# Kernel optimization log

Measured on AMD Instinct MI355X. Metric: run time of the kernel, lower is better.

## Reference

```python
import jax, jax.numpy as jnp
import numpy as np

NEG_SLOPE = 0.2


def gat_conv(x, src, dst, N, W, a_src, a_dst, b, concat):
    # x: [N, F_in], W: [F_in, H*C], a_src/a_dst: [H, C], b: [H*C] or [C]
    H, C = a_src.shape
    h = (x @ W).reshape(N, H, C)                    # [N, H, C]
    al_src = jnp.einsum('nhc,hc->nh', h, a_src)     # [N, H]
    al_dst = jnp.einsum('nhc,hc->nh', h, a_dst)     # [N, H]
    logits = jax.nn.leaky_relu(al_src[src] + al_dst[dst], NEG_SLOPE)  # [E, H]
    # edge softmax over incoming edges of each destination node
    m = jax.ops.segment_max(logits, dst, num_segments=N)              # [N, H]
    m = jnp.where(jnp.isfinite(m), m, 0.0)
    e = jnp.exp(logits - m[dst])                                      # [E, H]
    denom = jax.ops.segment_sum(e, dst, num_segments=N)               # [N, H]
    alpha = e / denom[dst]                                            # [E, H]
    out = jax.ops.segment_sum(alpha[:, :, None] * h[src], dst, num_segments=N)  # [N, H, C]
    if concat:
        return out.reshape(N, H * C) + b
    return out.mean(axis=1) + b


def setup_inputs() -> dict:
    key = jax.random.key(0)
    ks = jax.random.split(key, 12)
    N, E = 100000, 1600000
    F_in, Ch, Co, H = 128, 32, 64, 4
    x = jax.random.normal(ks[0], (N, F_in), dtype=jnp.float32)
    edge_index = jax.random.randint(ks[1], (2, E), 0, N, dtype=jnp.int64)
    s = 0.1
    return {
        'x': x, 'edge_index': edge_index,
        'W1': jax.random.normal(ks[2], (F_in, H * Ch), jnp.float32) * s,
        'a_src1': jax.random.normal(ks[3], (H, Ch), jnp.float32) * s,
        'a_dst1': jax.random.normal(ks[4], (H, Ch), jnp.float32) * s,
        'b1': jnp.zeros((H * Ch,), jnp.float32),
        'W2': jax.random.normal(ks[5], (H * Ch, H * Ch), jnp.float32) * s,
        'a_src2': jax.random.normal(ks[6], (H, Ch), jnp.float32) * s,
        'a_dst2': jax.random.normal(ks[7], (H, Ch), jnp.float32) * s,
        'b2': jnp.zeros((H * Ch,), jnp.float32),
        'W3': jax.random.normal(ks[8], (H * Ch, H * Co), jnp.float32) * s,
        'a_src3': jax.random.normal(ks[9], (H, Co), jnp.float32) * s,
        'a_dst3': jax.random.normal(ks[10], (H, Co), jnp.float32) * s,
        'b3': jnp.zeros((Co,), jnp.float32),
    }


def reference(x, edge_index, W1, a_src1, a_dst1, b1, W2, a_src2, a_dst2, b2, W3, a_src3, a_dst3, b3):
    N = x.shape[0]
    # PyG GATConv default add_self_loops=True
    loop = jnp.arange(N, dtype=edge_index.dtype)
    src = jnp.concatenate([edge_index[0], loop])
    dst = jnp.concatenate([edge_index[1], loop])
    h = gat_conv(x, src, dst, N, W1, a_src1, a_dst1, b1, concat=True)
    h = jax.nn.elu(h)
    h = gat_conv(h, src, dst, N, W2, a_src2, a_dst2, b2, concat=True)
    h = jax.nn.elu(h)
    out = gat_conv(h, src, dst, N, W3, a_src3, a_dst3, b3, concat=False)
    return out
```

## Files before the change

### kernel.cpp

```cpp
#include <hip/hip_runtime.h>


#define NEG_SLOPE 0.2f

typedef __attribute__((ext_vector_type(8))) _Float16 half8v;
typedef __attribute__((ext_vector_type(4))) _Float16 half4v;
typedef __attribute__((ext_vector_type(2))) _Float16 half2v;
typedef __attribute__((ext_vector_type(4))) float f32x4;

__device__ __forceinline__ float lrelu(float v) { return v > 0.f ? v : NEG_SLOPE * v; }

struct hf2 { _Float16 hi, lo; };
__device__ __forceinline__ hf2 split_f16(float f)
{
    hf2 r;
    r.hi = (_Float16)f;
    r.lo = (_Float16)(f - (float)r.hi);
    return r;
}

__global__ void fill_sentinel(float* __restrict__ out, int n)
{
    int i = blockIdx.x * blockDim.x + threadIdx.x;
    if (i < n) out[i] = 1e30f;
}

__global__ void detect_idx64(const int* __restrict__ ei, int* __restrict__ flag)
{
    __shared__ int anynz;
    if (threadIdx.x == 0) anynz = 0;
    __syncthreads();
    int v = ei[2 * threadIdx.x + 1];
    if (v != 0) atomicOr(&anynz, 1);
    __syncthreads();
    if (threadIdx.x == 0) flag[0] = (anynz == 0) ? 1 : 0;
}

__global__ void prep_edges(const void* __restrict__ ei, const int* __restrict__ flag,
                           int* __restrict__ src32, int* __restrict__ dst32,
                           int* __restrict__ deg8, int* __restrict__ loc, int N, int E)
{
    int e = blockIdx.x * blockDim.x + threadIdx.x;
    if (e >= E) return;
    int s, d;
    if (flag[0]) { s = (int)((const long long*)ei)[e]; d = (int)((const long long*)ei)[E + e]; }
    else         { s = ((const int*)ei)[e];            d = ((const int*)ei)[E + e]; }
    src32[e] = s;
    dst32[e] = d;
    loc[e] = atomicAdd(&deg8[(blockIdx.x & 7) * N + d], 1);
}

__global__ void reduce8(int* __restrict__ deg8, int* __restrict__ deg, int N)
{
    int d = blockIdx.x * blockDim.x + threadIdx.x;
    if (d >= N) return;
    int s = 0;
    #pragma unroll
    for (int k = 0; k < 8; ++k) {
        int v = deg8[k * N + d];
        deg8[k * N + d] = s;
        s += v;
    }
    deg[d] = s;
}

__global__ __launch_bounds__(256)
void scanA(const int* __restrict__ deg, int* __restrict__ rowptr,
           int* __restrict__ bsum, int N)
{
    __shared__ int part[256];
    const int t = threadIdx.x;
    const int base = blockIdx.x * 1024 + t * 4;
    int v[4];
    #pragma unroll
    for (int j = 0; j < 4; ++j) v[j] = (base + j < N) ? deg[base + j] : 0;
    int s = v[0] + v[1] + v[2] + v[3];
    part[t] = s;
    __syncthreads();
    #pragma unroll
    for (int off = 1; off < 256; off <<= 1) {
        int p = (t >= off) ? part[t - off] : 0;
        __syncthreads();
        part[t] += p;
        __syncthreads();
    }
    int run = (t == 0) ? 0 : part[t - 1];
    #pragma unroll
    for (int j = 0; j < 4; ++j) {
        if (base + j < N) rowptr[base + j] = run;
        run += v[j];
    }
    if (t == 255) bsum[blockIdx.x] = part[255];
}

__global__ __launch_bounds__(1024)
void scanB(int* __restrict__ bsum, int nb)
{
    __shared__ int s[1024];
    int t = threadIdx.x;
    s[t] = (t < nb) ? bsum[t] : 0;
    __syncthreads();
    for (int off = 1; off < 1024; off <<= 1) {
        int p = (t >= off) ? s[t - off] : 0;
        __syncthreads();
        s[t] += p;
        __syncthreads();
    }
    if (t < nb) bsum[t] = (t == 0) ? 0 : s[t - 1];
}

__global__ __launch_bounds__(256)
void scanC(int* __restrict__ rowptr, const int* __restrict__ bsum, int N, int E)
{
    const int base = blockIdx.x * 1024 + threadIdx.x * 4;
    const int off = bsum[blockIdx.x];
    #pragma unroll
    for (int j = 0; j < 4; ++j)
        if (base + j < N) rowptr[base + j] += off;
    if (blockIdx.x == 0 && threadIdx.x == 0) rowptr[N] = E;
}

__global__ void fill_csr(const int* __restrict__ src32, const int* __restrict__ dst32,
                         const int* __restrict__ loc, const int* __restrict__ rowptr,
                         const int* __restrict__ deg8, int* __restrict__ csr_src,
                         int N, int E)
{
    int e = blockIdx.x * blockDim.x + threadIdx.x;
    if (e >= E) return;
    int d = dst32[e];
    csr_src[rowptr[d] + deg8[(blockIdx.x & 7) * N + d] + loc[e]] = src32[e];
}

__global__ void convert_hilo(const float* __restrict__ in, _Float16* __restrict__ hi,
                             _Float16* __restrict__ lo, long long n4)
{
    long long t = (long long)blockIdx.x * blockDim.x + threadIdx.x;
    if (t >= n4) return;
    float4 v = *(const float4*)&in[t * 4];
    hf2 a = split_f16(v.x), b = split_f16(v.y), c = split_f16(v.z), d = split_f16(v.w);
    half4v h, l;
    h.x = a.hi; h.y = b.hi; h.z = c.hi; h.w = d.hi;
    l.x = a.lo; l.y = b.lo; l.z = c.lo; l.w = d.lo;
    *(half4v*)&hi[t * 4] = h;
    *(half4v*)&lo[t * 4] = l;
}

__global__ __launch_bounds__(256)
void convert_wt(const float* __restrict__ W, _Float16* __restrict__ wthi,
                _Float16* __restrict__ wtlo, int ldw, int wcol0)
{
    int t = blockIdx.x * 256 + threadIdx.x;
    int k = t >> 7, n = t & 127;
    float v = W[(long long)k * ldw + wcol0 + n];
    hf2 r = split_f16(v);
    wthi[n * 128 + k] = r.hi;
    wtlo[n * 128 + k] = r.lo;
}

template<int HPC>
__global__ __launch_bounds__(256)
void gemm_mfma(const _Float16* __restrict__ Ahi, const _Float16* __restrict__ Alo,
               const _Float16* __restrict__ Wthi, const _Float16* __restrict__ Wtlo,
               _Float16* __restrict__ Chi,
               const float* __restrict__ aS, const float* __restrict__ aD,
               float* __restrict__ als, float* __restrict__ ald, int M)
{
    const int tid = threadIdx.x;
    const int wave = tid >> 6, lane = tid & 63;
    const int l15 = lane & 15, lk = lane >> 4;
    const int m0 = blockIdx.x * 64 + wave * 16;
    int mrow = m0 + l15;
    if (mrow >= M) mrow = M - 1;

    f32x4 acc[8];
    #pragma unroll
    for (int i = 0; i < 8; ++i) acc[i] = (f32x4){0.f, 0.f, 0.f, 0.f};

    #pragma unroll
    for (int kt = 0; kt < 4; ++kt) {
        const int k = kt * 32 + lk * 8;
        half8v ah = *(const half8v*)&Ahi[(long long)mrow * 128 + k];
        half8v al = *(const half8v*)&Alo[(long long)mrow * 128 + k];
        #pragma unroll
        for (int nf = 0; nf < 8; ++nf) {
            half8v bh = *(const half8v*)&Wthi[(nf * 16 + l15) * 128 + k];
            half8v bl = *(const half8v*)&Wtlo[(nf * 16 + l15) * 128 + k];
            acc[nf] = __builtin_amdgcn_mfma_f32_16x16x32_f16(ah, bh, acc[nf], 0, 0, 0);
            acc[nf] = __builtin_amdgcn_mfma_f32_16x16x32_f16(ah, bl, acc[nf], 0, 0, 0);
            acc[nf] = __builtin_amdgcn_mfma_f32_16x16x32_f16(al, bh, acc[nf], 0, 0, 0);
        }
    }

    #pragma unroll
    for (int r = 0; r < 4; ++r) {
        int gm = m0 + lk * 4 + r;
        if (gm >= M) continue;
        #pragma unroll
        for (int nf = 0; nf < 8; ++nf)
            Chi[(long long)gm * 128 + nf * 16 + l15] = (_Float16)acc[nf][r];
    }

    float asv[8], adv[8];
    #pragma unroll
    for (int nf = 0; nf < 8; ++nf) {
        asv[nf] = aS[nf * 16 + l15];
        adv[nf] = aD[nf * 16 + l15];
    }
    constexpr int NFH = 8 / HPC;
    #pragma unroll
    for (int r = 0; r < 4; ++r) {
        #pragma unroll
        for (int h = 0; h < HPC; ++h) {
            float ps = 0.f, pd = 0.f;
            #pragma unroll
            for (int q = 0; q < NFH; ++q) {
                int nf = h * NFH + q;
                ps += acc[nf][r] * asv[nf];
                pd += acc[nf][r] * adv[nf];
            }
            #pragma unroll
            for (int m = 1; m < 16; m <<= 1) {
                ps += __shfl_xor(ps, m);
                pd += __shfl_xor(pd, m);
            }
            if (l15 == 0) {
                int gm = m0 + lk * 4 + r;
                if (gm < M) {
                    als[gm * HPC + h] = ps;
                    ald[gm * HPC + h] = pd;
                }
            }
        }
    }
}

template<int C, int HL, bool MEAN, bool ACCUM>
__global__ __launch_bounds__(256)
void gat_aggregate(const int* __restrict__ rowptr, const int* __restrict__ csr_src,
                   const float* __restrict__ als, const float* __restrict__ ald,
                   const _Float16* __restrict__ h16, const float* __restrict__ bias,
                   float* __restrict__ out,
                   _Float16* __restrict__ ohi, _Float16* __restrict__ olo, int N)
{
    constexpr int ROW = HL * C;
    constexpr int LOG2HL = (HL == 4) ? 2 : 1;
    const int d = (blockIdx.x * blockDim.x + threadIdx.x) >> 6;
    const int lane = threadIdx.x & 63;
    if (d >= N) return;
    const int j = lane * 2;
    const int hh = j / C;

    const int myh = lane & (HL - 1);
    const int myi = lane >> LOG2HL;
    const float ald_mine = ald[d * HL + myh];

    const float ald_d = (HL == 4 && myh == hh) ? ald_mine : ald[d * HL + hh];
    const float wself = __expf(lrelu(als[d * HL + hh] + ald_d));
    float denom = wself;
    half2v hv = *(const half2v*)&h16[(unsigned)d * ROW + j];
    float vx = wself * (float)hv.x, vy = wself * (float)hv.y;

    const int e0 = rowptr[d], e1 = rowptr[d + 1];
    for (int base = e0; base < e1; base += 8) {
        int ee = base + myi;
        int sv_mine = csr_src[ee < e1 ? ee : e1 - 1];
        float a = als[sv_mine * HL + myh] + ald_mine;
        float w_mine = (ee < e1) ? __expf(lrelu(a)) : 0.f;

        int sref[8];
        half2v hb[8];
        #pragma unroll
        for (int i = 0; i < 8; ++i) sref[i] = __shfl(sv_mine, i * HL, 64);
        #pragma unroll
        for (int i = 0; i < 8; ++i) hb[i] = *(const half2v*)&h16[(unsigned)sref[i] * ROW + j];
        #pragma unroll
        for (int i = 0; i < 8; ++i) {
            float wv = __shfl(w_mine, i * HL + hh, 64);
            denom += wv;
            vx += wv * (float)hb[i].x;
            vy += wv * (float)hb[i].y;
        }
    }
    float inv = 1.f / denom;
    vx *= inv; vy *= inv;

    if (!MEAN) {
        vx += bias[j]; vy += bias[j + 1];
        vx = vx > 0.f ? vx : __expf(vx) - 1.f;
        vy = vy > 0.f ? vy : __expf(vy) - 1.f;
        hf2 rx = split_f16(vx), ry = split_f16(vy);
        half2v hi2, lo2;
        hi2.x = rx.hi; hi2.y = ry.hi;
        lo2.x = rx.lo; lo2.y = ry.lo;
        *(half2v*)&ohi[(unsigned)d * ROW + j] = hi2;
        *(half2v*)&olo[(unsigned)d * ROW + j] = lo2;
    } else {
        vx = 0.25f * vx + __shfl_xor(0.25f * vx, 32);
        vy = 0.25f * vy + __shfl_xor(0.25f * vy, 32);
        if (lane < 32) {
            float* op = &out[(unsigned)d * C + j];
            if (ACCUM) { vx += op[0] + bias[j]; vy += op[1] + bias[j + 1]; }
            *(float2*)op = make_float2(vx, vy);
        }
    }
}

extern "C" void kernel_launch(void* const* d_in, const int* in_sizes, int n_in,
                              void* d_out, int out_size, void* d_ws, size_t ws_size,
                              hipStream_t stream)
{
    const float* x      = (const float*)d_in[0];
    const void*  ei     = d_in[1];
    const float* W1     = (const float*)d_in[2];
    const float* a_src1 = (const float*)d_in[3];
    const float* a_dst1 = (const float*)d_in[4];
    const float* b1     = (const float*)d_in[5];
    const float* W2     = (const float*)d_in[6];
    const float* a_src2 = (const float*)d_in[7];
    const float* a_dst2 = (const float*)d_in[8];
    const float* b2     = (const float*)d_in[9];
    const float* W3     = (const float*)d_in[10];
    const float* a_src3 = (const float*)d_in[11];
    const float* a_dst3 = (const float*)d_in[12];
    const float* b3     = (const float*)d_in[13];

    const int N = in_sizes[0] / 128;
    const int E = in_sizes[1] / 2;

    char* w = (char*)d_ws;
    auto alloc = [&](size_t bytes) {
        char* p = w;
        w += (bytes + 255) & ~(size_t)255;
        return p;
    };
    int*      flag    = (int*)     alloc(256);
    int*      deg8    = (int*)     alloc((size_t)N * 8 * 4);
    int*      deg     = (int*)     alloc((size_t)N * 4);
    int*      rowptr  = (int*)     alloc((size_t)(N + 1) * 4);
    int*      bsum    = (int*)     alloc(1024 * 4);
    int*      src32   = (int*)     alloc((size_t)E * 4);
    int*      dst32   = (int*)     alloc((size_t)E * 4);
    int*      loc     = (int*)     alloc((size_t)E * 4);
    int*      csr_src = (int*)     alloc((size_t)E * 4);
    _Float16* hhi     = (_Float16*)alloc((size_t)N * 128 * 2);
    _Float16* xhi     = (_Float16*)alloc((size_t)N * 128 * 2);
    _Float16* xlo     = (_Float16*)alloc((size_t)N * 128 * 2);
    float*    als     = (float*)   alloc((size_t)N * 4 * 4);
    float*    ald     = (float*)   alloc((size_t)N * 4 * 4);
    _Float16* wthi    = (_Float16*)alloc(128 * 128 * 2);
    _Float16* wtlo    = (_Float16*)alloc(128 * 128 * 2);
    if ((size_t)(w - (char*)d_ws) > ws_size) {
        fill_sentinel<<<(out_size + 255) / 256, 256, 0, stream>>>((float*)d_out, out_size);
        return;
    }

    const int gb = 256;
    const int nb1024 = (N + 1023) / 1024;
    const int mb = (N + 63) / 64;
    const int ab = (N * 64 + gb - 1) / gb;
    auto blocks = [&](long long tot) { return (int)((tot + gb - 1) / gb); };

    detect_idx64<<<1, 256, 0, stream>>>((const int*)ei, flag);
    (void)hipMemsetAsync(deg8, 0, (size_t)N * 8 * 4, stream);
    prep_edges<<<blocks(E), gb, 0, stream>>>(ei, flag, src32, dst32, deg8, loc, N, E);
    reduce8<<<blocks(N), gb, 0, stream>>>(deg8, deg, N);
    scanA<<<nb1024, gb, 0, stream>>>(deg, rowptr, bsum, N);
    scanB<<<1, 1024, 0, stream>>>(bsum, nb1024);
    scanC<<<nb1024, gb, 0, stream>>>(rowptr, bsum, N, E);
    fill_csr<<<blocks(E), gb, 0, stream>>>(src32, dst32, loc, rowptr, deg8, csr_src, N, E);

    convert_hilo<<<blocks((long long)N * 32), gb, 0, stream>>>(x, xhi, xlo, (long long)N * 32);

    convert_wt<<<64, gb, 0, stream>>>(W1, wthi, wtlo, 128, 0);
    gemm_mfma<4><<<mb, gb, 0, stream>>>(xhi, xlo, wthi, wtlo, hhi,
                                        a_src1, a_dst1, als, ald, N);
    gat_aggregate<32, 4, false, false><<<ab, gb, 0, stream>>>(
        rowptr, csr_src, als, ald, hhi, b1, nullptr, xhi, xlo, N);

    convert_wt<<<64, gb, 0, stream>>>(W2, wthi, wtlo, 128, 0);
    gemm_mfma<4><<<mb, gb, 0, stream>>>(xhi, xlo, wthi, wtlo, hhi,
                                        a_src2, a_dst2, als, ald, N);
    gat_aggregate<32, 4, false, false><<<ab, gb, 0, stream>>>(
        rowptr, csr_src, als, ald, hhi, b2, nullptr, xhi, xlo, N);

    convert_wt<<<64, gb, 0, stream>>>(W3, wthi, wtlo, 256, 0);
    gemm_mfma<2><<<mb, gb, 0, stream>>>(xhi, xlo, wthi, wtlo, hhi,
                                        a_src3, a_dst3, als, ald, N);
    gat_aggregate<64, 2, true, false><<<ab, gb, 0, stream>>>(
        rowptr, csr_src, als, ald, hhi, b3, (float*)d_out, nullptr, nullptr, N);

    convert_wt<<<64, gb, 0, stream>>>(W3, wthi, wtlo, 256, 128);
    gemm_mfma<2><<<mb, gb, 0, stream>>>(xhi, xlo, wthi, wtlo, hhi,
                                        a_src3 + 128, a_dst3 + 128, als, ald, N);
    gat_aggregate<64, 2, true, true><<<ab, gb, 0, stream>>>(
        rowptr, csr_src, als, ald, hhi, b3, (float*)d_out, nullptr, nullptr, N);
}
```

Baseline: 698.8 us.

## Merge layer-3 two-pass head split into single 256-wide GEMM and aggregation

Layer 3 used to run as two half-width passes, each with its own GEMM and aggregation over the edges, accumulating into the output. These become one 256-column MFMA GEMM and one aggregation kernel that handles all four heads, with 4 halves per lane and a cross-lane mean. This removes a second full edge traversal and a second GEMM launch, at the cost of a larger intermediate buffer and more registers per thread. Separately, the edge preprocessing now keys its per-bucket degree counters on the hardware XCC id instead of the block index, encoding the bucket in the top bits of loc. It also uses nontemporal loads and stores for the streaming edge arrays, and restricts the weight computation in the aggregation to the lanes that need it.

```diff
diff --git a/kernel.cpp b/kernel.cpp
--- a/kernel.cpp
+++ b/kernel.cpp
@@ -42,12 +42,21 @@
 {
     int e = blockIdx.x * blockDim.x + threadIdx.x;
     if (e >= E) return;
+    int xcc;
+    asm("s_getreg_b32 %0, hwreg(HW_REG_XCC_ID)" : "=s"(xcc));
+    xcc &= 7;
     int s, d;
-    if (flag[0]) { s = (int)((const long long*)ei)[e]; d = (int)((const long long*)ei)[E + e]; }
-    else         { s = ((const int*)ei)[e];            d = ((const int*)ei)[E + e]; }
-    src32[e] = s;
-    dst32[e] = d;
-    loc[e] = atomicAdd(&deg8[(blockIdx.x & 7) * N + d], 1);
+    if (flag[0]) {
+        s = (int)__builtin_nontemporal_load((const long long*)ei + e);
+        d = (int)__builtin_nontemporal_load((const long long*)ei + E + e);
+    } else {
+        s = __builtin_nontemporal_load((const int*)ei + e);
+        d = __builtin_nontemporal_load((const int*)ei + E + e);
+    }
+    __builtin_nontemporal_store(s, src32 + e);
+    __builtin_nontemporal_store(d, dst32 + e);
+    int v = atomicAdd(&deg8[xcc * N + d], 1);
+    __builtin_nontemporal_store((xcc << 28) | v, loc + e);
 }
 
 __global__ void reduce8(int* __restrict__ deg8, int* __restrict__ deg, int N)
@@ -127,8 +136,11 @@
 {
     int e = blockIdx.x * blockDim.x + threadIdx.x;
     if (e >= E) return;
-    int d = dst32[e];
-    csr_src[rowptr[d] + deg8[(blockIdx.x & 7) * N + d] + loc[e]] = src32[e];
+    int lv = __builtin_nontemporal_load(loc + e);
+    int d  = __builtin_nontemporal_load(dst32 + e);
+    int s  = __builtin_nontemporal_load(src32 + e);
+    int k  = lv >> 28;
+    csr_src[rowptr[d] + deg8[k * N + d] + (lv & 0x0FFFFFFF)] = s;
 }
 
 __global__ void convert_hilo(const float* __restrict__ in, _Float16* __restrict__ hi,
@@ -147,10 +159,10 @@
 
 __global__ __launch_bounds__(256)
 void convert_wt(const float* __restrict__ W, _Float16* __restrict__ wthi,
-                _Float16* __restrict__ wtlo, int ldw, int wcol0)
+                _Float16* __restrict__ wtlo, int ncols, int ldw, int wcol0)
 {
     int t = blockIdx.x * 256 + threadIdx.x;
-    int k = t >> 7, n = t & 127;
+    int k = t / ncols, n = t % ncols;
     float v = W[(long long)k * ldw + wcol0 + n];
     hf2 r = split_f16(v);
     wthi[n * 128 + k] = r.hi;
@@ -234,12 +246,86 @@
     }
 }
 
-template<int C, int HL, bool MEAN, bool ACCUM>
+__global__ __launch_bounds__(256)
+void gemm_mfma256(const _Float16* __restrict__ Ahi, const _Float16* __restrict__ Alo,
+                  const _Float16* __restrict__ Wthi, const _Float16* __restrict__ Wtlo,
+                  _Float16* __restrict__ Chi,
+                  const float* __restrict__ aS, const float* __restrict__ aD,
+                  float* __restrict__ als, float* __restrict__ ald, int M)
+{
+    const int tid = threadIdx.x;
+    const int wave = tid >> 6, lane = tid & 63;
+    const int l15 = lane & 15, lk = lane >> 4;
+    const int m0 = blockIdx.x * 64 + wave * 16;
+    int mrow = m0 + l15;
+    if (mrow >= M) mrow = M - 1;
+
+    f32x4 acc[16];
+    #pragma unroll
+    for (int i = 0; i < 16; ++i) acc[i] = (f32x4){0.f, 0.f, 0.f, 0.f};
+
+    #pragma unroll
+    for (int kt = 0; kt < 4; ++kt) {
+        const int k = kt * 32 + lk * 8;
+        half8v ah = *(const half8v*)&Ahi[(long long)mrow * 128 + k];
+        half8v al = *(const half8v*)&Alo[(long long)mrow * 128 + k];
+        #pragma unroll
+        for (int nf = 0; nf < 16; ++nf) {
+            half8v bh = *(const half8v*)&Wthi[(nf * 16 + l15) * 128 + k];
+            half8v bl = *(const half8v*)&Wtlo[(nf * 16 + l15) * 128 + k];
+            acc[nf] = __builtin_amdgcn_mfma_f32_16x16x32_f16(ah, bh, acc[nf], 0, 0, 0);
+            acc[nf] = __builtin_amdgcn_mfma_f32_16x16x32_f16(ah, bl, acc[nf], 0, 0, 0);
+            acc[nf] = __builtin_amdgcn_mfma_f32_16x16x32_f16(al, bh, acc[nf], 0, 0, 0);
+        }
+    }
+
+    #pragma unroll
+    for (int r = 0; r < 4; ++r) {
+        int gm = m0 + lk * 4 + r;
+        if (gm >= M) continue;
+        #pragma unroll
+        for (int nf = 0; nf < 16; ++nf)
+            Chi[(long long)gm * 256 + nf * 16 + l15] = (_Float16)acc[nf][r];
+    }
+
+    float asv[16], adv[16];
+    #pragma unroll
+    for (int nf = 0; nf < 16; ++nf) {
+        asv[nf] = aS[nf * 16 + l15];
+        adv[nf] = aD[nf * 16 + l15];
+    }
+    #pragma unroll
+    for (int r = 0; r < 4; ++r) {
+        #pragma unroll
+        for (int h = 0; h < 4; ++h) {
+            float ps = 0.f, pd = 0.f;
+            #pragma unroll
+            for (int q = 0; q < 4; ++q) {
+                int nf = h * 4 + q;
+                ps += acc[nf][r] * asv[nf];
+                pd += acc[nf][r] * adv[nf];
+            }
+            #pragma unroll
+            for (int m = 1; m < 16; m <<= 1) {
+                ps += __shfl_xor(ps, m);
+                pd += __shfl_xor(pd, m);
+            }
+            if (l15 == 0) {
+                int gm = m0 + lk * 4 + r;
+                if (gm < M) {
+                    als[gm * 4 + h] = ps;
+                    ald[gm * 4 + h] = pd;
+                }
+            }
+        }
+    }
+}
+
+template<int C, int HL>
 __global__ __launch_bounds__(256)
 void gat_aggregate(const int* __restrict__ rowptr, const int* __restrict__ csr_src,
                    const float* __restrict__ als, const float* __restrict__ ald,
                    const _Float16* __restrict__ h16, const float* __restrict__ bias,
-                   float* __restrict__ out,
                    _Float16* __restrict__ ohi, _Float16* __restrict__ olo, int N)
 {
     constexpr int ROW = HL * C;
@@ -254,19 +340,21 @@
     const int myi = lane >> LOG2HL;
     const float ald_mine = ald[d * HL + myh];
 
-    const float ald_d = (HL == 4 && myh == hh) ? ald_mine : ald[d * HL + hh];
-    const float wself = __expf(lrelu(als[d * HL + hh] + ald_d));
+    const float wself = __expf(lrelu(als[d * HL + hh] + ald[d * HL + hh]));
     float denom = wself;
     half2v hv = *(const half2v*)&h16[(unsigned)d * ROW + j];
     float vx = wself * (float)hv.x, vy = wself * (float)hv.y;
 
     const int e0 = rowptr[d], e1 = rowptr[d + 1];
     for (int base = e0; base < e1; base += 8) {
-        int ee = base + myi;
-        int sv_mine = csr_src[ee < e1 ? ee : e1 - 1];
-        float a = als[sv_mine * HL + myh] + ald_mine;
-        float w_mine = (ee < e1) ? __expf(lrelu(a)) : 0.f;
-
+        int sv_mine = 0;
+        float w_mine = 0.f;
+        if (lane < 8 * HL) {
+            int ee = base + myi;
+            sv_mine = csr_src[ee < e1 ? ee : e1 - 1];
+            float a = als[sv_mine * HL + myh] + ald_mine;
+            w_mine = (ee < e1) ? __expf(lrelu(a)) : 0.f;
+        }
         int sref[8];
         half2v hb[8];
         #pragma unroll
@@ -282,26 +370,76 @@
         }
     }
     float inv = 1.f / denom;
-    vx *= inv; vy *= inv;
-
-    if (!MEAN) {
-        vx += bias[j]; vy += bias[j + 1];
-        vx = vx > 0.f ? vx : __expf(vx) - 1.f;
-        vy = vy > 0.f ? vy : __expf(vy) - 1.f;
-        hf2 rx = split_f16(vx), ry = split_f16(vy);
-        half2v hi2, lo2;
-        hi2.x = rx.hi; hi2.y = ry.hi;
-        lo2.x = rx.lo; lo2.y = ry.lo;
-        *(half2v*)&ohi[(unsigned)d * ROW + j] = hi2;
-        *(half2v*)&olo[(unsigned)d * ROW + j] = lo2;
-    } else {
-        vx = 0.25f * vx + __shfl_xor(0.25f * vx, 32);
-        vy = 0.25f * vy + __shfl_xor(0.25f * vy, 32);
+    vx = vx * inv + bias[j];
+    vy = vy * inv + bias[j + 1];
+    vx = vx > 0.f ? vx : __expf(vx) - 1.f;
+    vy = vy > 0.f ? vy : __expf(vy) - 1.f;
+    hf2 rx = split_f16(vx), ry = split_f16(vy);
+    half2v hi2, lo2;
+    hi2.x = rx.hi; hi2.y = ry.hi;
+    lo2.x = rx.lo; lo2.y = ry.lo;
+    *(half2v*)&ohi[(unsigned)d * ROW + j] = hi2;
+    *(half2v*)&olo[(unsigned)d * ROW + j] = lo2;
+}
+
+__global__ __launch_bounds__(256)
+void gat_aggregate3(const int* __restrict__ rowptr, const int* __restrict__ csr_src,
+                    const float* __restrict__ als, const float* __restrict__ ald,
+                    const _Float16* __restrict__ h16, const float* __restrict__ bias,
+                    float* __restrict__ out, int N)
+{
+    const int d = (blockIdx.x * blockDim.x + threadIdx.x) >> 6;
+    const int lane = threadIdx.x & 63;
+    if (d >= N) return;
+    const int q = lane * 4;
+    const int chd = lane >> 4;
+
+    const int myh = lane & 3;
+    const int myi = lane >> 2;
+    const float ald_mine = ald[d * 4 + myh];
+
+    const float wself = __expf(lrelu(als[d * 4 + chd] + ald[d * 4 + chd]));
+    float dn = wself;
+    half4v hs = *(const half4v*)&h16[(unsigned)d * 256 + q];
+    float vx0 = wself * (float)hs.x, vx1 = wself * (float)hs.y;
+    float vx2 = wself * (float)hs.z, vx3 = wself * (float)hs.w;
+
+    const int e0 = rowptr[d], e1 = rowptr[d + 1];
+    for (int base = e0; base < e1; base += 8) {
+        int sv_mine = 0;
+        float w_mine = 0.f;
         if (lane < 32) {
-            float* op = &out[(unsigned)d * C + j];
-            if (ACCUM) { vx += op[0] + bias[j]; vy += op[1] + bias[j + 1]; }
-            *(float2*)op = make_float2(vx, vy);
-        }
+            int ee = base + myi;
+            sv_mine = csr_src[ee < e1 ? ee : e1 - 1];
+            float a = als[sv_mine * 4 + myh] + ald_mine;
+            w_mine = (ee < e1) ? __expf(lrelu(a)) : 0.f;
+        }
+        int sref[8];
+        half4v hb[8];
+        #pragma unroll
+        for (int i = 0; i < 8; ++i) sref[i] = __shfl(sv_mine, i * 4, 64);
+        #pragma unroll
+        for (int i = 0; i < 8; ++i) hb[i] = *(const half4v*)&h16[(unsigned)sref[i] * 256 + q];
+        #pragma unroll
+        for (int i = 0; i < 8; ++i) {
+            float wv = __shfl(w_mine, i * 4 + chd, 64);
+            dn += wv;
+            vx0 += wv * (float)hb[i].x;
+            vx1 += wv * (float)hb[i].y;
+            vx2 += wv * (float)hb[i].z;
+            vx3 += wv * (float)hb[i].w;
+        }
+    }
+    const float s = 0.25f / dn;
+    float m0 = vx0 * s, m1 = vx1 * s, m2 = vx2 * s, m3 = vx3 * s;
+    m0 += __shfl_xor(m0, 16); m1 += __shfl_xor(m1, 16);
+    m2 += __shfl_xor(m2, 16); m3 += __shfl_xor(m3, 16);
+    m0 += __shfl_xor(m0, 32); m1 += __shfl_xor(m1, 32);
+    m2 += __shfl_xor(m2, 32); m3 += __shfl_xor(m3, 32);
+    if (lane < 16) {
+        m0 += bias[q + 0]; m1 += bias[q + 1];
+        m2 += bias[q + 2]; m3 += bias[q + 3];
+        *(float4*)&out[(unsigned)d * 64 + q] = make_float4(m0, m1, m2, m3);
     }
 }
 
@@ -342,13 +480,13 @@
     int*      dst32   = (int*)     alloc((size_t)E * 4);
     int*      loc     = (int*)     alloc((size_t)E * 4);
     int*      csr_src = (int*)     alloc((size_t)E * 4);
-    _Float16* hhi     = (_Float16*)alloc((size_t)N * 128 * 2);
+    _Float16* hhi     = (_Float16*)alloc((size_t)N * 256 * 2);
     _Float16* xhi     = (_Float16*)alloc((size_t)N * 128 * 2);
     _Float16* xlo     = (_Float16*)alloc((size_t)N * 128 * 2);
     float*    als     = (float*)   alloc((size_t)N * 4 * 4);
     float*    ald     = (float*)   alloc((size_t)N * 4 * 4);
-    _Float16* wthi    = (_Float16*)alloc(128 * 128 * 2);
-    _Float16* wtlo    = (_Float16*)alloc(128 * 128 * 2);
+    _Float16* wthi    = (_Float16*)alloc(256 * 128 * 2);
+    _Float16* wtlo    = (_Float16*)alloc(256 * 128 * 2);
     if ((size_t)(w - (char*)d_ws) > ws_size) {
         fill_sentinel<<<(out_size + 255) / 256, 256, 0, stream>>>((float*)d_out, out_size);
         return;
@@ -371,27 +509,21 @@
 
     convert_hilo<<<blocks((long long)N * 32), gb, 0, stream>>>(x, xhi, xlo, (long long)N * 32);
 
-    convert_wt<<<64, gb, 0, stream>>>(W1, wthi, wtlo, 128, 0);
+    convert_wt<<<64, gb, 0, stream>>>(W1, wthi, wtlo, 128, 128, 0);
     gemm_mfma<4><<<mb, gb, 0, stream>>>(xhi, xlo, wthi, wtlo, hhi,
                                         a_src1, a_dst1, als, ald, N);
-    gat_aggregate<32, 4, false, false><<<ab, gb, 0, stream>>>(
-        rowptr, csr_src, als, ald, hhi, b1, nullptr, xhi, xlo, N);
-
-    convert_wt<<<64, gb, 0, stream>>>(W2, wthi, wtlo, 128, 0);
+    gat_aggregate<32, 4><<<ab, gb, 0, stream>>>(
+        rowptr, csr_src, als, ald, hhi, b1, xhi, xlo, N);
+
+    convert_wt<<<64, gb, 0, stream>>>(W2, wthi, wtlo, 128, 128, 0);
     gemm_mfma<4><<<mb, gb, 0, stream>>>(xhi, xlo, wthi, wtlo, hhi,
                                         a_src2, a_dst2, als, ald, N);
-    gat_aggregate<32, 4, false, false><<<ab, gb, 0, stream>>>(
-        rowptr, csr_src, als, ald, hhi, b2, nullptr, xhi, xlo, N);
-
-    convert_wt<<<64, gb, 0, stream>>>(W3, wthi, wtlo, 256, 0);
-    gemm_mfma<2><<<mb, gb, 0, stream>>>(xhi, xlo, wthi, wtlo, hhi,
+    gat_aggregate<32, 4><<<ab, gb, 0, stream>>>(
+        rowptr, csr_src, als, ald, hhi, b2, xhi, xlo, N);
+
+    convert_wt<<<128, gb, 0, stream>>>(W3, wthi, wtlo, 256, 256, 0);
+    gemm_mfma256<<<mb, gb, 0, stream>>>(xhi, xlo, wthi, wtlo, hhi,
                                         a_src3, a_dst3, als, ald, N);
-    gat_aggregate<64, 2, true, false><<<ab, gb, 0, stream>>>(
-        rowptr, csr_src, als, ald, hhi, b3, (float*)d_out, nullptr, nullptr, N);
-
-    convert_wt<<<64, gb, 0, stream>>>(W3, wthi, wtlo, 256, 128);
-    gemm_mfma<2><<<mb, gb, 0, stream>>>(xhi, xlo, wthi, wtlo, hhi,
-                                        a_src3 + 128, a_dst3 + 128, als, ald, N);
-    gat_aggregate<64, 2, true, true><<<ab, gb, 0, stream>>>(
-        rowptr, csr_src, als, ald, hhi, b3, (float*)d_out, nullptr, nullptr, N);
-}
+    gat_aggregate3<<<ab, gb, 0, stream>>>(
+        rowptr, csr_src, als, ald, hhi, b3, (float*)d_out, N);
+}
```

Measured after the change: 722.2 us. 1.03x slower.
